# Kernel tuning notes

Measured on AMD Instinct MI355X. Metric: run time of the kernel, lower is better.

Reference implementation:

```python
import jax, jax.numpy as jnp
import numpy as np

D_IN = 768
D_MODEL = 768
NUM_HEADS = 12
DEPTH = D_MODEL // NUM_HEADS


def setup_inputs() -> dict:
    key = jax.random.key(0)
    ks = jax.random.split(key, 9)
    B, N = 2, 2048
    s_in = 1.0 / np.sqrt(D_IN)
    s_md = 1.0 / np.sqrt(D_MODEL)
    return {
        "x": jax.random.normal(ks[0], (B, N, D_IN), dtype=jnp.float32),
        "wq": jax.random.normal(ks[1], (D_IN, D_MODEL), dtype=jnp.float32) * s_in,
        "bq": jax.random.normal(ks[2], (D_MODEL,), dtype=jnp.float32) * 0.02,
        "wk": jax.random.normal(ks[3], (D_IN, D_MODEL), dtype=jnp.float32) * s_in,
        "bk": jax.random.normal(ks[4], (D_MODEL,), dtype=jnp.float32) * 0.02,
        "wv": jax.random.normal(ks[5], (D_IN, D_MODEL), dtype=jnp.float32) * s_in,
        "bv": jax.random.normal(ks[6], (D_MODEL,), dtype=jnp.float32) * 0.02,
        "wo": jax.random.normal(ks[7], (D_MODEL, D_MODEL), dtype=jnp.float32) * s_md,
        "bo": jax.random.normal(ks[8], (D_MODEL,), dtype=jnp.float32) * 0.02,
    }


def reference(x, wq, bq, wk, bk, wv, bv, wo, bo):
    B, N, _ = x.shape
    H, D = NUM_HEADS, DEPTH
    # project and split heads: [B,N,H,D] -> [B,H,N,D]
    q = (x @ wq + bq).reshape(B, N, H, D).transpose(0, 2, 1, 3)
    k = (x @ wk + bk).reshape(B, N, H, D).transpose(0, 2, 1, 3)
    v = (x @ wv + bv).reshape(B, N, H, D).transpose(0, 2, 1, 3)
    scale = 1.0 / jnp.sqrt(jnp.asarray(D, dtype=q.dtype))
    attn = jnp.einsum('bhnd,bhmd->bhnm', q, k) * scale  # [B,H,N,N]
    attn = jax.nn.softmax(attn, axis=-1)
    z = jnp.einsum('bhnm,bhmd->bhnd', attn, v)
    z = z.transpose(0, 2, 1, 3).reshape(B, N, H * D)
    return z @ wo + bo
```

## Files before the change

### kernel.cpp

```cpp
#include <hip/hip_runtime.h>
#include <hip/hip_bf16.h>
#include <math.h>

#define NH 12
#define DH 64
#define BB 2
#define NN 2048
#define DM 768

typedef short v8s __attribute__((ext_vector_type(8)));
typedef float v4f __attribute__((ext_vector_type(4)));

__device__ __forceinline__ unsigned short f2bf(float f) {
    union { float f; unsigned u; } x; x.f = f;
    unsigned r = x.u + 0x7fffu + ((x.u >> 16) & 1u);
    return (unsigned short)(r >> 16);
}

__device__ __forceinline__ int cvtpk(float lo, float hi2) {
    int r;
    asm("v_cvt_pk_bf16_f32 %0, %1, %2" : "=v"(r) : "v"(lo), "v"(hi2));
    return r;
}

__device__ __forceinline__ void glds16(const void* g, void* l) {
    __builtin_amdgcn_global_load_lds((const __attribute__((address_space(1))) void*)g,
                                     (__attribute__((address_space(3))) void*)l, 16, 0, 0);
}

__global__ __launch_bounds__(256) void cast_x_k(const float* __restrict__ in,
                                                unsigned short* __restrict__ out, int n) {
    int i = (blockIdx.x * 256 + threadIdx.x) * 4;
    if (i >= n) return;
    float4 v = *(const float4*)(in + i);
    ushort4 o;
    o.x = f2bf(v.x); o.y = f2bf(v.y); o.z = f2bf(v.z); o.w = f2bf(v.w);
    *(ushort4*)(out + i) = o;
}

__global__ __launch_bounds__(256) void cast_wT_k(const float* __restrict__ w0, const float* __restrict__ w1,
                                                 const float* __restrict__ w2, const float* __restrict__ w3,
                                                 unsigned short* __restrict__ o0, unsigned short* __restrict__ o1,
                                                 unsigned short* __restrict__ o2, unsigned short* __restrict__ o3) {
    __shared__ unsigned short t[64][65];
    const float* in; unsigned short* out;
    switch (blockIdx.y) {
        case 0: in = w0; out = o0; break;
        case 1: in = w1; out = o1; break;
        case 2: in = w2; out = o2; break;
        default: in = w3; out = o3; break;
    }
    int kt = blockIdx.x / 12, ct = blockIdx.x % 12;
    int rr = threadIdx.x >> 4, cc = threadIdx.x & 15;
#pragma unroll
    for (int it = 0; it < 4; it++) {
        int row = kt * 64 + it * 16 + rr;
        int col = ct * 64 + cc * 4;
        float4 v = *(const float4*)(in + row * 768 + col);
        t[it * 16 + rr][cc * 4 + 0] = f2bf(v.x);
        t[it * 16 + rr][cc * 4 + 1] = f2bf(v.y);
        t[it * 16 + rr][cc * 4 + 2] = f2bf(v.z);
        t[it * 16 + rr][cc * 4 + 3] = f2bf(v.w);
    }
    __syncthreads();
#pragma unroll
    for (int it = 0; it < 4; it++) {
        int c_l = it * 16 + rr;
        int k_l = cc * 4;
        ushort4 o;
        o.x = t[k_l + 0][c_l];
        o.y = t[k_l + 1][c_l];
        o.z = t[k_l + 2][c_l];
        o.w = t[k_l + 3][c_l];
        *(ushort4*)(out + (ct * 64 + c_l) * 768 + kt * 64 + k_l) = o;
    }
}

__global__ __launch_bounds__(512) void qkv_gemm_k(
    const unsigned short* __restrict__ xb,
    const unsigned short* __restrict__ wqT, const unsigned short* __restrict__ wkT,
    const unsigned short* __restrict__ wvT,
    const float* __restrict__ bq, const float* __restrict__ bk, const float* __restrict__ bv,
    unsigned short* __restrict__ q, unsigned short* __restrict__ k, unsigned short* __restrict__ vT) {
    __shared__ unsigned short Abuf[3][128 * 32];
    __shared__ unsigned short Bbuf[3][128 * 32];

    int ctile = blockIdx.x;
    int mtile = blockIdx.y;
    int mat = ctile / 6;
    int col0 = (ctile % 6) * 128;
    const unsigned short* Bsrc = (mat == 0) ? wqT : ((mat == 1) ? wkT : wvT);
    const float* bias = (mat == 0) ? bq : ((mat == 1) ? bk : bv);

    int tid = threadIdx.x;
    int w = tid >> 6, l = tid & 63;
    int q16 = l & 15, g = l >> 4;
    int wr = w >> 2, wc = w & 3;

    int srow = tid >> 2;
    int ss = tid & 3;
    int c16s = ss ^ ((srow >> 1) & 3);

    auto stage = [&](int tt, int buf) {
        int k0 = tt * 32;
        glds16(xb + (mtile * 128 + srow) * 768 + k0 + (c16s << 3),
               (char*)&Abuf[buf][0] + tid * 16);
        glds16(Bsrc + (col0 + srow) * 768 + k0 + (c16s << 3),
               (char*)&Bbuf[buf][0] + tid * 16);
    };

    v4f zero = {0.f, 0.f, 0.f, 0.f};
    v4f acc[4][2];
#pragma unroll
    for (int i = 0; i < 4; i++)
#pragma unroll
        for (int j = 0; j < 2; j++) acc[i][j] = zero;

    stage(0, 0);
    stage(1, 1);
    asm volatile("s_waitcnt vmcnt(2)" ::: "memory");
    __builtin_amdgcn_s_barrier();
    asm volatile("" ::: "memory");

    int rd = 0;
    for (int tt = 0; tt < 24; ++tt) {
        int st = rd + 2; if (st >= 3) st -= 3;
        if (tt + 2 < 24) stage(tt + 2, st);
        const char* Ab = (const char*)&Abuf[rd][0];
        const char* Bb = (const char*)&Bbuf[rd][0];
        v8s af[4], bf[2];
#pragma unroll
        for (int f = 0; f < 4; f++) {
            int arow = wr * 64 + f * 16 + q16;
            af[f] = *(const v8s*)(Ab + arow * 64 + ((g ^ ((arow >> 1) & 3)) << 4));
        }
#pragma unroll
        for (int j = 0; j < 2; j++) {
            int brow = wc * 32 + j * 16 + q16;
            bf[j] = *(const v8s*)(Bb + brow * 64 + ((g ^ ((brow >> 1) & 3)) << 4));
        }
        __builtin_amdgcn_s_setprio(1);
#pragma unroll
        for (int i = 0; i < 4; i++)
#pragma unroll
            for (int j = 0; j < 2; j++)
                acc[i][j] = __builtin_amdgcn_mfma_f32_16x16x32_bf16(af[i], bf[j], acc[i][j], 0, 0, 0);
        __builtin_amdgcn_s_setprio(0);
        asm volatile("s_waitcnt vmcnt(2)" ::: "memory");
        __builtin_amdgcn_s_barrier();
        asm volatile("" ::: "memory");
        rd = (rd + 1 == 3) ? 0 : rd + 1;
    }

    const float QSCL = 0.125f * 1.44269504088896340736f;
#pragma unroll
    for (int i = 0; i < 4; i++)
#pragma unroll
        for (int j = 0; j < 2; j++)
#pragma unroll
            for (int r = 0; r < 4; r++) {
                int gr = mtile * 128 + wr * 64 + i * 16 + 4 * g + r;
                int gcl = col0 + wc * 32 + j * 16 + q16;
                int b = gr / NN, n = gr % NN;
                int h = gcl / DH, d = gcl % DH;
                int bh = b * NH + h;
                float v = acc[i][j][r] + bias[gcl];
                if (mat == 0)      q[(bh * NN + n) * DH + d]  = f2bf(v * QSCL);
                else if (mat == 1) k[(bh * NN + n) * DH + d]  = f2bf(v);
                else               vT[(bh * DH + d) * NN + n] = f2bf(v);
            }
}

__global__ __launch_bounds__(512) void attn_k(
    const unsigned short* __restrict__ q, const unsigned short* __restrict__ k,
    const unsigned short* __restrict__ vT, unsigned short* __restrict__ z) {
    __shared__ __align__(16) char Kb[2][2][4096];
    __shared__ __align__(16) char Vb[2][2][4096];
    __shared__ unsigned short plds[8][16][32];

    int bh = blockIdx.x % 24;
    int qt = blockIdx.x / 24;
    int b = bh / NH, h = bh % NH;
    int tid = threadIdx.x;
    int w = tid >> 6, l = tid & 63;
    int q16 = l & 15, g = l >> 4;
    int ws = w & 3, hf = w >> 2;

    const unsigned short* qp = q + (size_t)bh * NN * DH;
    const unsigned short* kp = k + (size_t)bh * NN * DH;
    const unsigned short* vp = vT + (size_t)bh * DH * NN;
    int qrow = qt * 64 + ws * 16 + q16;

    v8s qf0 = *(const v8s*)(qp + qrow * DH + 8 * g);
    v8s qf1 = *(const v8s*)(qp + qrow * DH + 32 + 8 * g);

    v8s ones;
#pragma unroll
    for (int i = 0; i < 8; i++) ones[i] = (short)0x3F80;

    int hf_s = tid >> 8;
    int s8 = tid & 255;
    int row_s = s8 >> 3, sl = s8 & 7;
    int kc16 = (sl ^ (row_s & 7)) & 7;
    int vj = sl ^ (row_s & 7);
    int vd = row_s + ((vj >> 2) << 5);
    int vkw = vj & 3;

    auto stage = [&](int t, int buf) {
        int kv0 = hf_s * (NN / 2) + t * 32;
        glds16(kp + (kv0 + row_s) * DH + (kc16 << 3), &Kb[hf_s][buf][s8 * 16]);
        glds16(vp + (size_t)vd * NN + kv0 + vkw * 8, &Vb[hf_s][buf][s8 * 16]);
    };

    v4f zero = {0.f, 0.f, 0.f, 0.f};
    float mrow = -INFINITY;
    v4f o[4];
    v4f osum = zero;
#pragma unroll
    for (int dt = 0; dt < 4; dt++) o[dt] = zero;

    stage(0, 0);
    __syncthreads();

    for (int t = 0; t < 32; ++t) {
        int cur = t & 1;
        if (t + 1 < 32) stage(t + 1, cur ^ 1);

        const char* kb = &Kb[hf][cur][0];
        const char* vb = &Vb[hf][cur][0];

        v4f st[2];
#pragma unroll
        for (int ct = 0; ct < 2; ct++) {
            int krow = ct * 16 + q16;
            v8s kf0 = *(const v8s*)(kb + krow * 128 + ((g ^ (krow & 7)) << 4));
            v8s kf1 = *(const v8s*)(kb + krow * 128 + (((4 + g) ^ (krow & 7)) << 4));
            __builtin_amdgcn_s_setprio(1);
            st[ct] = __builtin_amdgcn_mfma_f32_16x16x32_bf16(kf0, qf0, zero, 0, 0, 0);
            st[ct] = __builtin_amdgcn_mfma_f32_16x16x32_bf16(kf1, qf1, st[ct], 0, 0, 0);
            __builtin_amdgcn_s_setprio(0);
        }

        float ma = fmaxf(fmaxf(st[0][0], st[0][1]), st[0][2]);
        float mb = fmaxf(fmaxf(st[0][3], st[1][0]), st[1][1]);
        float vmax = fmaxf(fmaxf(ma, mb), fmaxf(st[1][2], st[1][3]));
        vmax = fmaxf(vmax, __shfl_xor(vmax, 16));
        vmax = fmaxf(vmax, __shfl_xor(vmax, 32));

        if (!__all(vmax <= mrow + 8.f)) {
            float mn = fmaxf(mrow, vmax);
            float sc = exp2f(mrow - mn);
#pragma unroll
            for (int dt = 0; dt < 4; dt++)
#pragma unroll
                for (int r = 0; r < 4; r++) o[dt][r] *= sc;
            osum[0] *= sc;
            mrow = mn;
        }

#pragma unroll
        for (int ct = 0; ct < 2; ct++) {
            float p0 = exp2f(st[ct][0] - mrow);
            float p1 = exp2f(st[ct][1] - mrow);
            float p2 = exp2f(st[ct][2] - mrow);
            float p3 = exp2f(st[ct][3] - mrow);
            union { int i[2]; short4 s; } u;
            u.i[0] = cvtpk(p0, p1);
            u.i[1] = cvtpk(p2, p3);
            *(short4*)(&plds[w][q16][ct * 16 + 4 * g]) = u.s;
        }

        v8s pf0 = *(const v8s*)(&plds[w][q16][8 * g]);

        osum = __builtin_amdgcn_mfma_f32_16x16x32_bf16(ones, pf0, osum, 0, 0, 0);

        __builtin_amdgcn_s_setprio(1);
#pragma unroll
        for (int dt = 0; dt < 4; dt++) {
            int dcol = dt * 16 + q16;
            int rr = dcol & 31;
            int sl2 = (((dcol >> 5) << 2) + g) ^ (rr & 7);
            v8s vf = *(const v8s*)(vb + rr * 128 + (sl2 << 4));
            o[dt] = __builtin_amdgcn_mfma_f32_16x16x32_bf16(vf, pf0, o[dt], 0, 0, 0);
        }
        __builtin_amdgcn_s_setprio(0);
        __syncthreads();
    }

    float* po = (float*)&Kb[0][0][0];
    float* pm = (float*)&Vb[0][0][0];
    float* pl = pm + 64;
    int row = ws * 16 + q16;

    if (hf == 1) {
#pragma unroll
        for (int dt = 0; dt < 4; dt++)
#pragma unroll
            for (int r = 0; r < 4; r++)
                po[row * 64 + dt * 16 + 4 * g + r] = o[dt][r];
        if (g == 0) { pm[row] = mrow; pl[row] = osum[0]; }
    }
    __syncthreads();
    if (hf == 0) {
        float m1 = pm[row], l1 = pl[row];
        float ms = fmaxf(mrow, m1);
        float a0 = exp2f(mrow - ms), a1 = exp2f(m1 - ms);
        float inv = 1.f / (osum[0] * a0 + l1 * a1);
        int n = qt * 64 + ws * 16 + q16;
#pragma unroll
        for (int dt = 0; dt < 4; dt++) {
            short4 s4;
            s4.x = (short)f2bf((o[dt][0] * a0 + po[row * 64 + dt * 16 + 4 * g + 0] * a1) * inv);
            s4.y = (short)f2bf((o[dt][1] * a0 + po[row * 64 + dt * 16 + 4 * g + 1] * a1) * inv);
            s4.z = (short)f2bf((o[dt][2] * a0 + po[row * 64 + dt * 16 + 4 * g + 2] * a1) * inv);
            s4.w = (short)f2bf((o[dt][3] * a0 + po[row * 64 + dt * 16 + 4 * g + 3] * a1) * inv);
            *(short4*)(&z[((size_t)(b * NN + n)) * DM + h * DH + dt * 16 + 4 * g]) = s4;
        }
    }
}

__global__ __launch_bounds__(512) void out_gemm_k(
    const unsigned short* __restrict__ zb, const unsigned short* __restrict__ woT,
    const float* __restrict__ bo, float* __restrict__ out) {
    __shared__ unsigned short Abuf[3][128 * 32];
    __shared__ unsigned short Bbuf[3][128 * 32];

    int ctile = blockIdx.x;
    int mtile = blockIdx.y;
    int col0 = ctile * 128;

    int tid = threadIdx.x;
    int w = tid >> 6, l = tid & 63;
    int q16 = l & 15, g = l >> 4;
    int wr = w >> 2, wc = w & 3;

    int srow = tid >> 2;
    int ss = tid & 3;
    int c16s = ss ^ ((srow >> 1) & 3);

    auto stage = [&](int tt, int buf) {
        int k0 = tt * 32;
        glds16(zb + (mtile * 128 + srow) * 768 + k0 + (c16s << 3),
               (char*)&Abuf[buf][0] + tid * 16);
        glds16(woT + (col0 + srow) * 768 + k0 + (c16s << 3),
               (char*)&Bbuf[buf][0] + tid * 16);
    };

    v4f zero = {0.f, 0.f, 0.f, 0.f};
    v4f acc[4][2];
#pragma unroll
    for (int i = 0; i < 4; i++)
#pragma unroll
        for (int j = 0; j < 2; j++) acc[i][j] = zero;

    stage(0, 0);
    stage(1, 1);
    asm volatile("s_waitcnt vmcnt(2)" ::: "memory");
    __builtin_amdgcn_s_barrier();
    asm volatile("" ::: "memory");

    int rd = 0;
    for (int tt = 0; tt < 24; ++tt) {
        int st = rd + 2; if (st >= 3) st -= 3;
        if (tt + 2 < 24) stage(tt + 2, st);
        const char* Ab = (const char*)&Abuf[rd][0];
        const char* Bb = (const char*)&Bbuf[rd][0];
        v8s af[4], bf[2];
#pragma unroll
        for (int f = 0; f < 4; f++) {
            int arow = wr * 64 + f * 16 + q16;
            af[f] = *(const v8s*)(Ab + arow * 64 + ((g ^ ((arow >> 1) & 3)) << 4));
        }
#pragma unroll
        for (int j = 0; j < 2; j++) {
            int brow = wc * 32 + j * 16 + q16;
            bf[j] = *(const v8s*)(Bb + brow * 64 + ((g ^ ((brow >> 1) & 3)) << 4));
        }
        __builtin_amdgcn_s_setprio(1);
#pragma unroll
        for (int i = 0; i < 4; i++)
#pragma unroll
            for (int j = 0; j < 2; j++)
                acc[i][j] = __builtin_amdgcn_mfma_f32_16x16x32_bf16(af[i], bf[j], acc[i][j], 0, 0, 0);
        __builtin_amdgcn_s_setprio(0);
        asm volatile("s_waitcnt vmcnt(2)" ::: "memory");
        __builtin_amdgcn_s_barrier();
        asm volatile("" ::: "memory");
        rd = (rd + 1 == 3) ? 0 : rd + 1;
    }

#pragma unroll
    for (int i = 0; i < 4; i++)
#pragma unroll
        for (int j = 0; j < 2; j++)
#pragma unroll
            for (int r = 0; r < 4; r++) {
                int gr = mtile * 128 + wr * 64 + i * 16 + 4 * g + r;
                int gc = col0 + wc * 32 + j * 16 + q16;
                out[gr * 768 + gc] = acc[i][j][r] + bo[gc];
            }
}

extern "C" void kernel_launch(void* const* d_in, const int* in_sizes, int n_in,
                              void* d_out, int out_size, void* d_ws, size_t ws_size,
                              hipStream_t stream) {
    const float* x  = (const float*)d_in[0];
    const float* wq = (const float*)d_in[1];
    const float* bq = (const float*)d_in[2];
    const float* wk = (const float*)d_in[3];
    const float* bk = (const float*)d_in[4];
    const float* wv = (const float*)d_in[5];
    const float* bv = (const float*)d_in[6];
    const float* wo = (const float*)d_in[7];
    const float* bo = (const float*)d_in[8];
    float* out = (float*)d_out;

    const int NX = BB * NN * DM;
    const int NW = 768 * 768;

    unsigned short* wsp = (unsigned short*)d_ws;
    unsigned short* xb  = wsp;
    unsigned short* wqT = xb + NX;
    unsigned short* wkT = wqT + NW;
    unsigned short* wvT = wkT + NW;
    unsigned short* woT = wvT + NW;
    unsigned short* qb  = woT + NW;
    unsigned short* kb  = qb + NX;
    unsigned short* vTb = kb + NX;
    unsigned short* zb  = vTb + NX;

    cast_x_k<<<NX / (256 * 4), 256, 0, stream>>>(x, xb, NX);
    cast_wT_k<<<dim3(144, 4), 256, 0, stream>>>(wq, wk, wv, wo, wqT, wkT, wvT, woT);
    qkv_gemm_k<<<dim3(18, 32), 512, 0, stream>>>(xb, wqT, wkT, wvT, bq, bk, bv, qb, kb, vTb);
    attn_k<<<BB * NH * (NN / 64), 512, 0, stream>>>(qb, kb, vTb, zb);
    out_gemm_k<<<dim3(6, 32), 512, 0, stream>>>(zb, woT, bo, out);
}
```

Baseline: 132.6 us.

## Fuse cast kernels, swizzle GEMM block order, pad attention P LDS buffer

```diff
diff --git a/kernel.cpp b/kernel.cpp
--- a/kernel.cpp
+++ b/kernel.cpp
@@ -28,29 +28,32 @@
                                      (__attribute__((address_space(3))) void*)l, 16, 0, 0);
 }
 
-__global__ __launch_bounds__(256) void cast_x_k(const float* __restrict__ in,
-                                                unsigned short* __restrict__ out, int n) {
-    int i = (blockIdx.x * 256 + threadIdx.x) * 4;
-    if (i >= n) return;
-    float4 v = *(const float4*)(in + i);
-    ushort4 o;
-    o.x = f2bf(v.x); o.y = f2bf(v.y); o.z = f2bf(v.z); o.w = f2bf(v.w);
-    *(ushort4*)(out + i) = o;
-}
-
-__global__ __launch_bounds__(256) void cast_wT_k(const float* __restrict__ w0, const float* __restrict__ w1,
-                                                 const float* __restrict__ w2, const float* __restrict__ w3,
-                                                 unsigned short* __restrict__ o0, unsigned short* __restrict__ o1,
-                                                 unsigned short* __restrict__ o2, unsigned short* __restrict__ o3) {
+__global__ __launch_bounds__(256) void cast_fused_k(
+    const float* __restrict__ x, unsigned short* __restrict__ xb,
+    const float* __restrict__ w0, const float* __restrict__ w1,
+    const float* __restrict__ w2, const float* __restrict__ w3,
+    unsigned short* __restrict__ o0, unsigned short* __restrict__ o1,
+    unsigned short* __restrict__ o2, unsigned short* __restrict__ o3) {
     __shared__ unsigned short t[64][65];
+    int bid = blockIdx.x;
+    if (bid < 3072) {
+        int i = (bid * 256 + threadIdx.x) * 4;
+        float4 v = *(const float4*)(x + i);
+        ushort4 o;
+        o.x = f2bf(v.x); o.y = f2bf(v.y); o.z = f2bf(v.z); o.w = f2bf(v.w);
+        *(ushort4*)(xb + i) = o;
+        return;
+    }
+    int idx = bid - 3072;
+    int m = idx / 144, xt = idx % 144;
     const float* in; unsigned short* out;
-    switch (blockIdx.y) {
+    switch (m) {
         case 0: in = w0; out = o0; break;
         case 1: in = w1; out = o1; break;
         case 2: in = w2; out = o2; break;
         default: in = w3; out = o3; break;
     }
-    int kt = blockIdx.x / 12, ct = blockIdx.x % 12;
+    int kt = xt / 12, ct = xt % 12;
     int rr = threadIdx.x >> 4, cc = threadIdx.x & 15;
 #pragma unroll
     for (int it = 0; it < 4; it++) {
@@ -85,8 +88,10 @@
     __shared__ unsigned short Abuf[3][128 * 32];
     __shared__ unsigned short Bbuf[3][128 * 32];
 
-    int ctile = blockIdx.x;
-    int mtile = blockIdx.y;
+    int lin = blockIdx.x;
+    int swz = (lin & 7) * 72 + (lin >> 3);
+    int ctile = swz % 18;
+    int mtile = swz / 18;
     int mat = ctile / 6;
     int col0 = (ctile % 6) * 128;
     const unsigned short* Bsrc = (mat == 0) ? wqT : ((mat == 1) ? wkT : wvT);
@@ -176,7 +181,7 @@
     const unsigned short* __restrict__ vT, unsigned short* __restrict__ z) {
     __shared__ __align__(16) char Kb[2][2][4096];
     __shared__ __align__(16) char Vb[2][2][4096];
-    __shared__ unsigned short plds[8][16][32];
+    __shared__ unsigned short plds[8][16][36];
 
     int bh = blockIdx.x % 24;
     int qt = blockIdx.x / 24;
@@ -325,8 +330,10 @@
     __shared__ unsigned short Abuf[3][128 * 32];
     __shared__ unsigned short Bbuf[3][128 * 32];
 
-    int ctile = blockIdx.x;
-    int mtile = blockIdx.y;
+    int lin = blockIdx.x;
+    int swz = (lin & 7) * 24 + (lin >> 3);
+    int ctile = swz % 6;
+    int mtile = swz / 6;
     int col0 = ctile * 128;
 
     int tid = threadIdx.x;
@@ -429,9 +436,8 @@
     unsigned short* vTb = kb + NX;
     unsigned short* zb  = vTb + NX;
 
-    cast_x_k<<<NX / (256 * 4), 256, 0, stream>>>(x, xb, NX);
-    cast_wT_k<<<dim3(144, 4), 256, 0, stream>>>(wq, wk, wv, wo, wqT, wkT, wvT, woT);
-    qkv_gemm_k<<<dim3(18, 32), 512, 0, stream>>>(xb, wqT, wkT, wvT, bq, bk, bv, qb, kb, vTb);
+    cast_fused_k<<<3648, 256, 0, stream>>>(x, xb, wq, wk, wv, wo, wqT, wkT, wvT, woT);
+    qkv_gemm_k<<<576, 512, 0, stream>>>(xb, wqT, wkT, wvT, bq, bk, bv, qb, kb, vTb);
     attn_k<<<BB * NH * (NN / 64), 512, 0, stream>>>(qb, kb, vTb, zb);
-    out_gemm_k<<<dim3(6, 32), 512, 0, stream>>>(zb, woT, bo, out);
-}
+    out_gemm_k<<<192, 512, 0, stream>>>(zb, woT, bo, out);
+}
```

After: 116.6 us. -12.1%, faster.
